# Optimization experiments

Hardware: AMD Instinct MI355X
Metric: run time of the kernel (lower is better)

Reference implementation:

```python
import jax, jax.numpy as jnp
import numpy as np
import math

B, N, IN_DIMS, OUT_DIMS = 128, 4096, 128, 64
LN_EPS = 1e-5


def setup_inputs() -> dict:
    key = jax.random.key(0)
    k_x, k_w, k_b = jax.random.split(key, 3)
    bound = math.sqrt(1.0 / (IN_DIMS + OUT_DIMS))
    x = jax.random.normal(k_x, (B, N, IN_DIMS), dtype=jnp.float32)
    w1 = jax.random.uniform(k_w, (IN_DIMS, OUT_DIMS, N), minval=-bound, maxval=bound, dtype=jnp.float32)
    b1 = jax.random.uniform(k_b, (1, N, OUT_DIMS), minval=-bound, maxval=bound, dtype=jnp.float32)
    gamma = jnp.ones((IN_DIMS,), dtype=jnp.float32)   # LayerNorm elementwise affine weight
    beta = jnp.zeros((IN_DIMS,), dtype=jnp.float32)   # LayerNorm elementwise affine bias
    T = jnp.asarray(1.0, dtype=jnp.float32)           # learnable temperature scalar
    return {"x": x, "gamma": gamma, "beta": beta, "w1": w1, "b1": b1, "T": T}


def _layernorm(x, gamma, beta):
    # normalize over last dim (in_dims), biased variance as in torch LayerNorm
    mu = jnp.mean(x, axis=-1, keepdims=True)
    var = jnp.mean(jnp.square(x - mu), axis=-1, keepdims=True)
    return (x - mu) * jax.lax.rsqrt(var + LN_EPS) * gamma + beta


def reference(x, gamma, beta, w1, b1, T):
    # dropout(p=0) is Identity
    xn = _layernorm(x, gamma, beta)
    # Faithful to torch.einsum('bni,iog->bno', x, w1): the g (N) axis of w1
    # is absent from the output, hence summed over -> effective weight w1.sum(-1).
    out = jnp.einsum('bni,io->bno', xn, jnp.sum(w1, axis=-1)) + b1
    out = out * T
    # out_dims != 1, so no squeeze
    return out
```

## Files before the change

### kernel.cpp

```cpp
#include <hip/hip_runtime.h>
#include <stdint.h>


constexpr int   Ndim = 4096;
constexpr int   IN   = 128;
constexpr int   OUT  = 64;
constexpr float EPS  = 1e-5f;

typedef __bf16 bf16x8 __attribute__((ext_vector_type(8)));
typedef unsigned short ushort8 __attribute__((ext_vector_type(8)));
typedef float f32x4 __attribute__((ext_vector_type(4)));
typedef float f32x2 __attribute__((ext_vector_type(2)));
typedef unsigned int u32x4 __attribute__((ext_vector_type(4)));

__device__ __forceinline__ unsigned short f2bf_rne(float f) {
    unsigned int u = __float_as_uint(f);
    u = (u + 0x7FFFu + ((u >> 16) & 1u)) >> 16;
    return (unsigned short)u;
}

__device__ __forceinline__ unsigned int cvt_pk_bf16(float lo, float hi) {
    unsigned int r;
    asm("v_cvt_pk_bf16_f32 %0, %1, %2" : "=v"(r) : "v"(lo), "v"(hi));
    return r;
}

__global__ __launch_bounds__(256) void reduce_w_kernel(
    const float* __restrict__ w1, float* __restrict__ Weff)
{
    const int p    = blockIdx.x * 4 + (threadIdx.x >> 6);
    const int lane = threadIdx.x & 63;
    const float4* w4 = (const float4*)(w1 + (long)p * Ndim);

    float s = 0.f;
    #pragma unroll
    for (int j = 0; j < 16; ++j) {
        float4 v = w4[j * 64 + lane];
        s += (v.x + v.y) + (v.z + v.w);
    }
    #pragma unroll
    for (int m = 1; m <= 32; m <<= 1) s += __shfl_xor(s, m);
    if (lane == 0) Weff[p] = s;
}

__global__ __launch_bounds__(256) void prep_kernel(
    const float* __restrict__ Weff,
    const float* __restrict__ gamma,
    const float* __restrict__ beta,
    const float* __restrict__ b1,
    const float* __restrict__ Tp,
    float* __restrict__ GwT, float* __restrict__ TBw,
    unsigned short* __restrict__ Wfrag,
    float* __restrict__ b1adj, int do_adj)
{
    const int tid = threadIdx.x;
    __shared__ float Ws[IN * OUT];
    __shared__ float gs[IN], bs[IN];
    __shared__ float redg[256], redb[256];
    __shared__ float Bws[OUT];
    const float Tv = Tp[0];

    #pragma unroll
    for (int k = 0; k < 32; ++k) Ws[k * 256 + tid] = Weff[k * 256 + tid];
    if (tid < IN) { gs[tid] = gamma[tid]; bs[tid] = beta[tid]; }
    __syncthreads();

    {
        const int o = tid & 63, grp = tid >> 6;
        float gw = 0.f, bw = 0.f;
        #pragma unroll
        for (int ii = 0; ii < 32; ++ii) {
            int i = grp * 32 + ii;
            float w = Ws[i * OUT + o];
            gw = fmaf(gs[i], w, gw);
            bw = fmaf(bs[i], w, bw);
        }
        redg[tid] = gw; redb[tid] = bw;
    }
    __syncthreads();
    if (tid < OUT) {
        float bwf = redb[tid] + redb[64 + tid] + redb[128 + tid] + redb[192 + tid];
        Bws[tid] = bwf;
        if (blockIdx.x == 0) {
            float gwf = redg[tid] + redg[64 + tid] + redg[128 + tid] + redg[192 + tid];
            GwT[tid] = Tv * gwf;
            TBw[tid] = Tv * bwf;
        }
    }
    __syncthreads();

    if (do_adj) {
        const float* src = b1 + (long)blockIdx.x * 64 * OUT;
        float*       dst = b1adj + (long)blockIdx.x * 64 * OUT;
        #pragma unroll
        for (int v = 0; v < 4; ++v) {
            int e = tid * 16 + v * 4;
            f32x4 t = *(const f32x4*)(src + e);
            #pragma unroll
            for (int j = 0; j < 4; ++j)
                t[j] = Tv * (t[j] + Bws[(e + j) & 63]);
            *(f32x4*)(dst + e) = t;
        }
    }

    if (blockIdx.x != 0) return;

    #pragma unroll
    for (int t = 0; t < 32; ++t) {
        int e    = t * 256 + tid;
        int j    = e & 7;
        int lane = (e >> 3) & 63;
        int pr   = e >> 9;
        int kt   = pr >> 2, nt = pr & 3;
        int k    = kt * 32 + ((lane >> 4) << 3) + j;
        int n    = nt * 16 + (lane & 15);
        Wfrag[e] = f2bf_rne(Tv * gs[k] * Ws[k * OUT + n]);
    }
}

constexpr int ROWS_PER_BLOCK = 256;

template<bool ADJ>
__global__ __launch_bounds__(256, 3) void fused_mfma_kernel(
    const float* __restrict__ x,
    const unsigned short* __restrict__ Wfrag,
    const float* __restrict__ GwT,
    const float* __restrict__ TBw,
    const float* __restrict__ b1a,
    const float* __restrict__ Tp,
    float* __restrict__ out)
{
    const int tid  = threadIdx.x;
    const int wave = tid >> 6;
    const int lane = tid & 63;
    const int q    = lane >> 4;
    const int mloc = lane & 15;

    bf16x8 bfr[4][4];
    const ushort8* wf8 = (const ushort8*)Wfrag;
    #pragma unroll
    for (int kt = 0; kt < 4; ++kt)
        #pragma unroll
        for (int nt = 0; nt < 4; ++nt) {
            ushort8 u = wf8[(kt * 4 + nt) * 64 + lane];
            bfr[kt][nt] = __builtin_bit_cast(bf16x8, u);
        }

    float GwTl[4], TBwl[4];
    #pragma unroll
    for (int nt = 0; nt < 4; ++nt) {
        GwTl[nt] = GwT[nt * 16 + mloc];
        TBwl[nt] = ADJ ? 0.f : TBw[nt * 16 + mloc];
    }
    const float Tv = ADJ ? 1.f : Tp[0];

    const long wave_row0 = (long)blockIdx.x * ROWS_PER_BLOCK + wave * 64;

    #pragma unroll
    for (int c = 0; c < 4; ++c) {
        const long row0 = wave_row0 + c * 16;

        const float* xr = x + (row0 + mloc) * IN + q * 8;
        f32x4 xv[8];
        #pragma unroll
        for (int kt = 0; kt < 4; ++kt) {
            xv[2 * kt]     = *(const f32x4*)(xr + kt * 32);
            xv[2 * kt + 1] = *(const f32x4*)(xr + kt * 32 + 4);
        }

        f32x2 sp = {0.f, 0.f}, qp = {0.f, 0.f};
        #pragma unroll
        for (int v = 0; v < 8; ++v) {
            f32x2 a = __builtin_shufflevector(xv[v], xv[v], 0, 1);
            f32x2 b = __builtin_shufflevector(xv[v], xv[v], 2, 3);
            sp += a;          sp += b;
            qp  = a * a + qp; qp  = b * b + qp;
        }
        float s  = sp[0] + sp[1];
        float s2 = qp[0] + qp[1];
        s  += __shfl_xor(s, 16);  s  += __shfl_xor(s, 32);
        s2 += __shfl_xor(s2, 16); s2 += __shfl_xor(s2, 32);
        float mu  = s * (1.f / IN);
        float var = fmaf(-mu, mu, s2 * (1.f / IN));
        float rs  = rsqrtf(var + EPS);
        float nb  = -rs * mu;

        bf16x8 af[4];
        #pragma unroll
        for (int kt = 0; kt < 4; ++kt) {
            u32x4 w;
            w[0] = cvt_pk_bf16(xv[2 * kt][0],     xv[2 * kt][1]);
            w[1] = cvt_pk_bf16(xv[2 * kt][2],     xv[2 * kt][3]);
            w[2] = cvt_pk_bf16(xv[2 * kt + 1][0], xv[2 * kt + 1][1]);
            w[3] = cvt_pk_bf16(xv[2 * kt + 1][2], xv[2 * kt + 1][3]);
            af[kt] = __builtin_bit_cast(bf16x8, w);
        }

        f32x4 acc[4] = {{0.f,0.f,0.f,0.f},{0.f,0.f,0.f,0.f},
                        {0.f,0.f,0.f,0.f},{0.f,0.f,0.f,0.f}};
        #pragma unroll
        for (int kt = 0; kt < 4; ++kt)
            #pragma unroll
            for (int nt = 0; nt < 4; ++nt)
                acc[nt] = __builtin_amdgcn_mfma_f32_16x16x32_bf16(
                              af[kt], bfr[kt][nt], acc[nt], 0, 0, 0);

        #pragma unroll
        for (int r = 0; r < 4; ++r) {
            int   rloc = q * 4 + r;
            float rsr  = __shfl(rs, rloc);
            float nbr  = __shfl(nb, rloc);
            long  row  = row0 + rloc;
            int   n    = (int)(row & (Ndim - 1));
            const float* brow = b1a + (long)n * OUT;
            #pragma unroll
            for (int nt = 0; nt < 4; ++nt) {
                int   o    = nt * 16 + mloc;
                float base = ADJ ? brow[o] : fmaf(Tv, brow[o], TBwl[nt]);
                float val  = fmaf(rsr, acc[nt][r], fmaf(nbr, GwTl[nt], base));
                out[row * OUT + o] = val;
            }
        }
    }
}

extern "C" void kernel_launch(void* const* d_in, const int* in_sizes, int n_in,
                              void* d_out, int out_size, void* d_ws, size_t ws_size,
                              hipStream_t stream)
{
    const float* x     = (const float*)d_in[0];
    const float* gamma = (const float*)d_in[1];
    const float* beta  = (const float*)d_in[2];
    const float* w1    = (const float*)d_in[3];
    const float* b1    = (const float*)d_in[4];
    const float* T     = (const float*)d_in[5];
    float*       out   = (float*)d_out;

    float*          ws    = (float*)d_ws;
    float*          Weff  = ws;
    float*          GwT   = ws + 8192;
    float*          TBw   = ws + 8256;
    unsigned short* Wfrag = (unsigned short*)(ws + 8320);
    float*          b1adj = ws + 12416;

    const size_t NEED = (size_t)(12416 + 262144) * sizeof(float);
    const bool   adj  = ws_size >= NEED;

    reduce_w_kernel<<<2048, 256, 0, stream>>>(w1, Weff);

    prep_kernel<<<adj ? 64 : 1, 256, 0, stream>>>(
        Weff, gamma, beta, b1, T, GwT, TBw, Wfrag, b1adj, adj ? 1 : 0);

    const long rows = 128L * 4096L;
    if (adj)
        fused_mfma_kernel<true ><<<rows / ROWS_PER_BLOCK, 256, 0, stream>>>(
            x, Wfrag, GwT, TBw, b1adj, T, out);
    else
        fused_mfma_kernel<false><<<rows / ROWS_PER_BLOCK, 256, 0, stream>>>(
            x, Wfrag, GwT, TBw, b1, T, out);
}
```

Baseline: 497.4 us.

## Swap MFMA operand order for row-contiguous float4 epilogue stores; build Wfrag in reduce

The MFMA operands are swapped so the weight fragment is the A operand and x the B operand. Each lane then holds four consecutive output columns of a single row, so the epilogue can use float4 loads of the bias and float4 stores of the output without per-row shuffles of the LayerNorm stats. Construction of the bf16 weight fragments moves into the reduction kernel, and the shared-memory staging of Weff in prep is dropped in favour of direct global reads. The aim is cheaper, wider global stores and less prep work, at the cost of scattered 2-byte writes in the reduction kernel.

```diff
diff --git a/kernel.cpp b/kernel.cpp
--- a/kernel.cpp
+++ b/kernel.cpp
@@ -26,7 +26,11 @@
 }
 
 __global__ __launch_bounds__(256) void reduce_w_kernel(
-    const float* __restrict__ w1, float* __restrict__ Weff)
+    const float* __restrict__ w1,
+    const float* __restrict__ gamma,
+    const float* __restrict__ Tp,
+    float* __restrict__ Weff,
+    unsigned short* __restrict__ Wfrag)
 {
     const int p    = blockIdx.x * 4 + (threadIdx.x >> 6);
     const int lane = threadIdx.x & 63;
@@ -40,7 +44,15 @@
     }
     #pragma unroll
     for (int m = 1; m <= 32; m <<= 1) s += __shfl_xor(s, m);
-    if (lane == 0) Weff[p] = s;
+    if (lane == 0) {
+        Weff[p] = s;
+        const int i  = p >> 6, o = p & 63;
+        const int kt = i >> 5, j = i & 7, hi = (i >> 3) & 3;
+        const int ot = o >> 4;
+        const int fl = hi * 16 + (o & 15);
+        Wfrag[(((kt * 4 + ot) * 64) + fl) * 8 + j] =
+            f2bf_rne(Tp[0] * gamma[i] * s);
+    }
 }
 
 __global__ __launch_bounds__(256) void prep_kernel(
@@ -50,18 +62,14 @@
     const float* __restrict__ b1,
     const float* __restrict__ Tp,
     float* __restrict__ GwT, float* __restrict__ TBw,
-    unsigned short* __restrict__ Wfrag,
     float* __restrict__ b1adj, int do_adj)
 {
     const int tid = threadIdx.x;
-    __shared__ float Ws[IN * OUT];
+    __shared__ float redg[256], redb[256];
     __shared__ float gs[IN], bs[IN];
-    __shared__ float redg[256], redb[256];
     __shared__ float Bws[OUT];
     const float Tv = Tp[0];
 
-    #pragma unroll
-    for (int k = 0; k < 32; ++k) Ws[k * 256 + tid] = Weff[k * 256 + tid];
     if (tid < IN) { gs[tid] = gamma[tid]; bs[tid] = beta[tid]; }
     __syncthreads();
 
@@ -71,7 +79,7 @@
         #pragma unroll
         for (int ii = 0; ii < 32; ++ii) {
             int i = grp * 32 + ii;
-            float w = Ws[i * OUT + o];
+            float w = Weff[i * OUT + o];
             gw = fmaf(gs[i], w, gw);
             bw = fmaf(bs[i], w, bw);
         }
@@ -101,20 +109,6 @@
                 t[j] = Tv * (t[j] + Bws[(e + j) & 63]);
             *(f32x4*)(dst + e) = t;
         }
-    }
-
-    if (blockIdx.x != 0) return;
-
-    #pragma unroll
-    for (int t = 0; t < 32; ++t) {
-        int e    = t * 256 + tid;
-        int j    = e & 7;
-        int lane = (e >> 3) & 63;
-        int pr   = e >> 9;
-        int kt   = pr >> 2, nt = pr & 3;
-        int k    = kt * 32 + ((lane >> 4) << 3) + j;
-        int n    = nt * 16 + (lane & 15);
-        Wfrag[e] = f2bf_rne(Tv * gs[k] * Ws[k * OUT + n]);
     }
 }
 
@@ -136,21 +130,25 @@
     const int q    = lane >> 4;
     const int mloc = lane & 15;
 
-    bf16x8 bfr[4][4];
+    bf16x8 wfr[4][4];
     const ushort8* wf8 = (const ushort8*)Wfrag;
     #pragma unroll
     for (int kt = 0; kt < 4; ++kt)
         #pragma unroll
-        for (int nt = 0; nt < 4; ++nt) {
-            ushort8 u = wf8[(kt * 4 + nt) * 64 + lane];
-            bfr[kt][nt] = __builtin_bit_cast(bf16x8, u);
-        }
-
-    float GwTl[4], TBwl[4];
-    #pragma unroll
-    for (int nt = 0; nt < 4; ++nt) {
-        GwTl[nt] = GwT[nt * 16 + mloc];
-        TBwl[nt] = ADJ ? 0.f : TBw[nt * 16 + mloc];
+        for (int ot = 0; ot < 4; ++ot) {
+            ushort8 u = wf8[(kt * 4 + ot) * 64 + lane];
+            wfr[kt][ot] = __builtin_bit_cast(bf16x8, u);
+        }
+
+    f32x4 GwTl[4];
+    #pragma unroll
+    for (int ot = 0; ot < 4; ++ot)
+        GwTl[ot] = *(const f32x4*)(GwT + ot * 16 + q * 4);
+    f32x4 TBwl[4];
+    if (!ADJ) {
+        #pragma unroll
+        for (int ot = 0; ot < 4; ++ot)
+            TBwl[ot] = *(const f32x4*)(TBw + ot * 16 + q * 4);
     }
     const float Tv = ADJ ? 1.f : Tp[0];
 
@@ -185,7 +183,7 @@
         float rs  = rsqrtf(var + EPS);
         float nb  = -rs * mu;
 
-        bf16x8 af[4];
+        bf16x8 xf[4];
         #pragma unroll
         for (int kt = 0; kt < 4; ++kt) {
             u32x4 w;
@@ -193,7 +191,7 @@
             w[1] = cvt_pk_bf16(xv[2 * kt][2],     xv[2 * kt][3]);
             w[2] = cvt_pk_bf16(xv[2 * kt + 1][0], xv[2 * kt + 1][1]);
             w[3] = cvt_pk_bf16(xv[2 * kt + 1][2], xv[2 * kt + 1][3]);
-            af[kt] = __builtin_bit_cast(bf16x8, w);
+            xf[kt] = __builtin_bit_cast(bf16x8, w);
         }
 
         f32x4 acc[4] = {{0.f,0.f,0.f,0.f},{0.f,0.f,0.f,0.f},
@@ -201,25 +199,24 @@
         #pragma unroll
         for (int kt = 0; kt < 4; ++kt)
             #pragma unroll
-            for (int nt = 0; nt < 4; ++nt)
-                acc[nt] = __builtin_amdgcn_mfma_f32_16x16x32_bf16(
-                              af[kt], bfr[kt][nt], acc[nt], 0, 0, 0);
-
-        #pragma unroll
-        for (int r = 0; r < 4; ++r) {
-            int   rloc = q * 4 + r;
-            float rsr  = __shfl(rs, rloc);
-            float nbr  = __shfl(nb, rloc);
-            long  row  = row0 + rloc;
-            int   n    = (int)(row & (Ndim - 1));
-            const float* brow = b1a + (long)n * OUT;
+            for (int ot = 0; ot < 4; ++ot)
+                acc[ot] = __builtin_amdgcn_mfma_f32_16x16x32_bf16(
+                              wfr[kt][ot], xf[kt], acc[ot], 0, 0, 0);
+
+        const long row  = row0 + mloc;
+        const int  n    = (int)(row & (Ndim - 1));
+        const float* brow = b1a + (long)n * OUT + q * 4;
+        float*       orow = out + row * OUT + q * 4;
+        #pragma unroll
+        for (int ot = 0; ot < 4; ++ot) {
+            f32x4 bv = *(const f32x4*)(brow + ot * 16);
+            f32x4 r;
             #pragma unroll
-            for (int nt = 0; nt < 4; ++nt) {
-                int   o    = nt * 16 + mloc;
-                float base = ADJ ? brow[o] : fmaf(Tv, brow[o], TBwl[nt]);
-                float val  = fmaf(rsr, acc[nt][r], fmaf(nbr, GwTl[nt], base));
-                out[row * OUT + o] = val;
+            for (int e = 0; e < 4; ++e) {
+                float base = ADJ ? bv[e] : fmaf(Tv, bv[e], TBwl[ot][e]);
+                r[e] = fmaf(rs, acc[ot][e], fmaf(nb, GwTl[ot][e], base));
             }
+            *(f32x4*)(orow + ot * 16) = r;
         }
     }
 }
@@ -246,10 +243,10 @@
     const size_t NEED = (size_t)(12416 + 262144) * sizeof(float);
     const bool   adj  = ws_size >= NEED;
 
-    reduce_w_kernel<<<2048, 256, 0, stream>>>(w1, Weff);
+    reduce_w_kernel<<<2048, 256, 0, stream>>>(w1, gamma, T, Weff, Wfrag);
 
     prep_kernel<<<adj ? 64 : 1, 256, 0, stream>>>(
-        Weff, gamma, beta, b1, T, GwT, TBw, Wfrag, b1adj, adj ? 1 : 0);
+        Weff, gamma, beta, b1, T, GwT, TBw, b1adj, adj ? 1 : 0);
 
     const long rows = 128L * 4096L;
     if (adj)
```

Result: no change. 503.0 us (+1.1%).
